# Optimization experiments

Hardware: AMD Instinct MI355X
Metric: run time of the kernel (lower is better)

Reference implementation:

```python
import jax, jax.numpy as jnp
import numpy as np

B, S, D, H = 2, 2048, 1024, 16
HD = D // H  # 64
SCALE = np.sqrt(HD).astype(np.float32)


def setup_inputs() -> dict:
    key = jax.random.key(0)
    k1, k2, k3, k4, k5, k6 = jax.random.split(key, 6)
    hidden_states = jax.random.normal(k1, (B, S, D), dtype=jnp.float32)
    attention_mask = jax.random.randint(k2, (B, 1, S, S), 0, 2) > 0  # bool
    std = 0.02
    W_qkv = jax.random.normal(k3, (D, 3 * D), dtype=jnp.float32) * std
    b_qkv = jnp.zeros((3 * D,), dtype=jnp.float32)
    W_dense = jax.random.normal(k4, (D, D), dtype=jnp.float32) * std
    b_dense = jnp.zeros((D,), dtype=jnp.float32)
    return {
        "hidden_states": hidden_states,
        "attention_mask": attention_mask,
        "W_qkv": W_qkv,
        "b_qkv": b_qkv,
        "W_dense": W_dense,
        "b_dense": b_dense,
    }


def reference(hidden_states, attention_mask, W_qkv, b_qkv, W_dense, b_dense):
    # fused QKV projection: [B,S,3D]
    qkv = hidden_states @ W_qkv + b_qkv
    q, k, v = jnp.split(qkv, 3, axis=-1)
    # split heads -> [B,H,S,hd]
    q = q.reshape(B, S, H, HD).transpose(0, 2, 1, 3)
    k = k.reshape(B, S, H, HD).transpose(0, 2, 1, 3)
    v = v.reshape(B, S, H, HD).transpose(0, 2, 1, 3)
    # scores [B,H,S,S]
    scores = jnp.einsum("bhqd,bhkd->bhqk", q, k) / SCALE
    scores = jnp.where(attention_mask, scores, jnp.float32(-50000.0))
    probs = jax.nn.softmax(scores, axis=-1)
    ctx = jnp.einsum("bhqk,bhkd->bhqd", probs, v)
    # merge heads -> [B,S,D]
    ctx = ctx.transpose(0, 2, 1, 3).reshape(B, S, D)
    return ctx @ W_dense + b_dense
```

## Files before the change

kernel.cpp:

```cpp
#include <hip/hip_runtime.h>
#include <stdint.h>

#define B_ 2
#define S_ 2048
#define D_ 1024
#define H_ 16
#define HD_ 64
#define D3_ 3072
#define KD_ 1024

typedef __attribute__((ext_vector_type(8))) __bf16 bf16x8;
typedef __attribute__((ext_vector_type(4))) float f32x4;
typedef __attribute__((ext_vector_type(16))) float f32x16;
typedef __attribute__((ext_vector_type(4))) unsigned int u32x4;

typedef const __attribute__((address_space(1))) unsigned int gu32_t;
typedef __attribute__((address_space(3))) unsigned int lu32_t;

static __device__ __forceinline__ unsigned short f2bf(float f) {
  unsigned int u = __float_as_uint(f);
  u += 0x7fffu + ((u >> 16) & 1u);
  return (unsigned short)(u >> 16);
}

static __device__ __forceinline__ void gll16(const unsigned short* g, unsigned short* l) {
  __builtin_amdgcn_global_load_lds((gu32_t*)(const void*)g, (lu32_t*)(void*)l, 16, 0, 0);
}

static __device__ __forceinline__ bf16x8 lds_read8(const unsigned short* p) {
  return *reinterpret_cast<const bf16x8*>(p);
}

static __device__ __forceinline__ unsigned int cvtpk(float lo, float hi) {
  unsigned int r;
  asm("v_cvt_pk_bf16_f32 %0, %1, %2" : "=v"(r) : "v"(lo), "v"(hi));
  return r;
}

static __device__ __forceinline__ void plswap(unsigned int& a, unsigned int& b) {
  asm("v_permlane32_swap_b32 %0, %1" : "+v"(a), "+v"(b));
}

static __device__ __forceinline__ void transpose32(const float* __restrict__ in,
                                                   unsigned short* __restrict__ out,
                                                   int K, int N, int bx, int by, int t,
                                                   float (*tsm)[33]) {
  const int k0 = by * 32, n0 = bx * 32;
  const int tx = t & 31, ty = t >> 5;
  #pragma unroll
  for (int j = 0; j < 32; j += 8) tsm[ty + j][tx] = in[(size_t)(k0 + ty + j) * N + n0 + tx];
  __syncthreads();
  #pragma unroll
  for (int j = 0; j < 32; j += 8) out[(size_t)(n0 + ty + j) * K + k0 + tx] = f2bf(tsm[tx][ty + j]);
}

__global__ void prep_kernel(const float* __restrict__ hidden, unsigned short* __restrict__ Xb,
                            const float* __restrict__ Wq, unsigned short* __restrict__ Wqt,
                            const void* __restrict__ mask,
                            unsigned long long* __restrict__ bits,
                            const float* __restrict__ Wd, unsigned short* __restrict__ Wdt) {
  __shared__ float tsm[32][33];
  __shared__ unsigned int red2[2];
  const int bid = blockIdx.x;
  const int t = threadIdx.x;
  if (bid < 4096) {
    const int i = (bid * 256 + t) * 4;
    float4 v = *reinterpret_cast<const float4*>(hidden + i);
    unsigned long long p = (unsigned long long)f2bf(v.x)
                         | ((unsigned long long)f2bf(v.y) << 16)
                         | ((unsigned long long)f2bf(v.z) << 32)
                         | ((unsigned long long)f2bf(v.w) << 48);
    *reinterpret_cast<unsigned long long*>(Xb + i) = p;
  } else if (bid < 7168) {
    const int bb = bid - 4096;
    transpose32(Wq, Wqt, KD_, D3_, bb % 96, bb / 96, t, tsm);
  } else if (bid < 8192) {
    if (t < 2) red2[t] = 0;
    __syncthreads();
    {
      const unsigned int* mw = (const unsigned int*)mask;
      unsigned int hb = 0, fl = 0;
      for (int i = t; i < 4096; i += 256) {
        unsigned int v = mw[i];
        hb |= (v & 0xFFFFFF00u);
        fl |= (v == 0x3F800000u) ? 1u : 0u;
      }
      atomicOr(&red2[0], hb);
      atomicOr(&red2[1], fl);
    }
    __syncthreads();
    const unsigned int mode = red2[1] ? 2u : (red2[0] ? 1u : 0u);
    const int lane = t & 63;
    const int nwaves = 1024 * 4;
    const int wid = ((bid - 7168) * 256 + t) >> 6;
    const int total = (B_ * S_ * S_) / 256;
    for (int wb = wid; wb < total; wb += nwaves) {
      const size_t base = (size_t)wb * 256 + lane;
      unsigned long long m0, m1, m2, m3;
      if (mode == 0) {
        const int* p = (const int*)mask;
        m0 = __ballot(p[base] != 0);       m1 = __ballot(p[base + 64] != 0);
        m2 = __ballot(p[base + 128] != 0); m3 = __ballot(p[base + 192] != 0);
      } else if (mode == 1) {
        const unsigned char* p = (const unsigned char*)mask;
        m0 = __ballot(p[base] != 0);       m1 = __ballot(p[base + 64] != 0);
        m2 = __ballot(p[base + 128] != 0); m3 = __ballot(p[base + 192] != 0);
      } else {
        const float* p = (const float*)mask;
        m0 = __ballot(p[base] != 0.f);       m1 = __ballot(p[base + 64] != 0.f);
        m2 = __ballot(p[base + 128] != 0.f); m3 = __ballot(p[base + 192] != 0.f);
      }
      if (lane < 4) {
        unsigned long long v = (lane & 1) ? m1 : m0;
        unsigned long long w2 = (lane & 1) ? m3 : m2;
        v = (lane & 2) ? w2 : v;
        bits[(size_t)wb * 4 + lane] = v;
      }
    }
  } else {
    const int bb = bid - 8192;
    transpose32(Wd, Wdt, D_, D_, bb & 31, bb >> 5, t, tsm);
  }
}

__global__ void tcvt_kernel(const float* __restrict__ in, unsigned short* __restrict__ out, int K, int N) {
  __shared__ float tsm[32][33];
  transpose32(in, out, K, N, blockIdx.x, blockIdx.y, threadIdx.x, tsm);
}

#define DSA256(BUF, MH, KC) \
  _Pragma("unroll") for (int fm_ = 0; fm_ < 4; ++fm_) \
    aq[fm_] = lds_read8(&Al[BUF][(wm * 128 + (MH) * 64 + fm_ * 16 + c16) * 64 + (KC)]);
#define DSB256(BUF, KC) \
  _Pragma("unroll") for (int fn_ = 0; fn_ < 3; ++fn_) \
    bq[fn_] = lds_read8(&Bl[BUF][(wn * 48 + fn_ * 16 + c16) * 64 + (KC)]);
#define MM256(MH) \
  __builtin_amdgcn_s_setprio(1); \
  _Pragma("unroll") for (int fm_ = 0; fm_ < 4; ++fm_) \
    _Pragma("unroll") for (int fn_ = 0; fn_ < 3; ++fn_) \
      acc[MH][fm_][fn_] = __builtin_amdgcn_mfma_f32_16x16x32_bf16(aq[fm_], bq[fn_], acc[MH][fm_][fn_], 0, 0, 0); \
  __builtin_amdgcn_s_setprio(0);
#define STA256(BUF, KT1) \
  _Pragma("unroll") for (int q_ = 0; q_ < 4; ++q_) \
    gll16(Ag + (size_t)(q_ * 64) * KD_ + (size_t)(KT1) * 64, &Al[BUF][q_ * 4096 + t * 8]);
#define STB256(BUF, KT1) \
  _Pragma("unroll") for (int q_ = 0; q_ < 3; ++q_) \
    gll16(Bg + (size_t)(q_ * 64) * KD_ + (size_t)(KT1) * 64, &Bl[BUF][q_ * 4096 + t * 8]);

__global__ __launch_bounds__(512, 2) void gemm256_kernel(
    const unsigned short* __restrict__ A,
    const unsigned short* __restrict__ Bt,
    const float* __restrict__ bias,
    unsigned short* __restrict__ Qh,
    unsigned short* __restrict__ Kh,
    unsigned short* __restrict__ Vt) {
  __shared__ unsigned short Al[2][16384];
  __shared__ unsigned short Bl[2][12288];
  const int t = threadIdx.x;
  const int lane = t & 63, w = t >> 6;
  const int g = lane >> 4, c16 = lane & 15;
  const int wm = w >> 2, wn = w & 3;

  const int wg = blockIdx.x;
  const int sw = (wg & 7) * 32 + (wg >> 3);
  const int by = sw >> 4, bx = sw & 15;
  const int m0 = by * 256, n0 = bx * 192;

  f32x4 acc[2][4][3];
  #pragma unroll
  for (int mh = 0; mh < 2; ++mh)
    #pragma unroll
    for (int fm = 0; fm < 4; ++fm)
      #pragma unroll
      for (int fn = 0; fn < 3; ++fn)
        #pragma unroll
        for (int r = 0; r < 4; ++r) acc[mh][fm][fn][r] = 0.f;

  const int srow = t >> 3;
  const int scb = (t & 7) ^ (srow & 7);
  const unsigned short* Ag = A + (size_t)(m0 + srow) * KD_ + scb * 8;
  const unsigned short* Bg = Bt + (size_t)(n0 + srow) * KD_ + scb * 8;

  const int kc0 = ((g ^ (c16 & 7)) * 8);
  const int kc1 = (((4 + g) ^ (c16 & 7)) * 8);

  bf16x8 aq[4], bq[3];

  STA256(0, 0); STB256(0, 0);
  __syncthreads();

  #pragma unroll 1
  for (int kt = 0; kt < 16; ++kt) {
    const int buf = kt & 1, nb = buf ^ 1;
    const bool st = kt < 15;
    DSA256(buf, 0, kc0); DSB256(buf, kc0);
    if (st) STA256(nb, kt + 1);
    MM256(0);
    DSA256(buf, 1, kc0);
    if (st) STB256(nb, kt + 1);
    MM256(1);
    DSA256(buf, 0, kc1); DSB256(buf, kc1);
    MM256(0);
    DSA256(buf, 1, kc1);
    MM256(1);
    __syncthreads();
  }

  #pragma unroll
  for (int mh = 0; mh < 2; ++mh) {
    #pragma unroll
    for (int fn = 0; fn < 3; ++fn) {
      const int n = n0 + wn * 48 + fn * 16 + c16;
      const float bv = bias[n];
      const int sel = n >> 10;
      const int hh = (n & 1023) >> 6;
      const int d = n & 63;
      #pragma unroll
      for (int fm = 0; fm < 4; ++fm) {
        const int m_b = m0 + wm * 128 + mh * 64 + fm * 16 + g * 4;
        const int b = m_b >> 11;
        const int s0 = m_b & 2047;
        const int bh = b * H_ + hh;
        if (sel == 2) {
          ushort4 pk;
          pk.x = f2bf(acc[mh][fm][fn][0] + bv);
          pk.y = f2bf(acc[mh][fm][fn][1] + bv);
          pk.z = f2bf(acc[mh][fm][fn][2] + bv);
          pk.w = f2bf(acc[mh][fm][fn][3] + bv);
          *reinterpret_cast<ushort4*>(&Vt[(size_t)(bh * HD_ + d) * S_ + s0]) = pk;
        } else {
          #pragma unroll
          for (int r = 0; r < 4; ++r) {
            const float v = acc[mh][fm][fn][r] + bv;
            if (sel == 0) Qh[(size_t)(bh * S_ + s0 + r) * HD_ + d] = f2bf(v * 0.18033688011112042f);
            else          Kh[(size_t)(bh * S_ + s0 + r) * HD_ + d] = f2bf(v);
          }
        }
      }
    }
  }
}

#define DDA(BUF, KC) \
  _Pragma("unroll") for (int i_ = 0; i_ < 4; ++i_) \
    aq[i_] = lds_read8(&Al[BUF][(wr * 64 + i_ * 16 + c16) * 64 + (KC)]);
#define DDB(BUF, KC) \
  _Pragma("unroll") for (int i_ = 0; i_ < 4; ++i_) \
    bq[i_] = lds_read8(&Bl[BUF][(wc * 64 + i_ * 16 + c16) * 64 + (KC)]);
#define DMM \
  __builtin_amdgcn_s_setprio(1); \
  _Pragma("unroll") for (int mi_ = 0; mi_ < 4; ++mi_) \
    _Pragma("unroll") for (int ni_ = 0; ni_ < 4; ++ni_) \
      acc[mi_][ni_] = __builtin_amdgcn_mfma_f32_16x16x32_bf16(aq[mi_], bq[ni_], acc[mi_][ni_], 0, 0, 0); \
  __builtin_amdgcn_s_setprio(0);
#define DSTA(BUF, KT1) \
  _Pragma("unroll") for (int q_ = 0; q_ < 4; ++q_) \
    gll16(Ag + (size_t)(q_ * 32) * KD_ + (size_t)(KT1) * 64, &Al[BUF][q_ * 2048 + t * 8]);
#define DSTB(BUF, KT1) \
  _Pragma("unroll") for (int q_ = 0; q_ < 4; ++q_) \
    gll16(Bg + (size_t)(q_ * 32) * KD_ + (size_t)(KT1) * 64, &Bl[BUF][q_ * 2048 + t * 8]);

__global__ __launch_bounds__(256, 2) void gemm128p_kernel(
    const unsigned short* __restrict__ A,
    const unsigned short* __restrict__ Bt,
    const float* __restrict__ bias,
    int Ndim,
    float* __restrict__ Out) {
  __shared__ unsigned short Al[2][8192];
  __shared__ unsigned short Bl[2][8192];
  const int t = threadIdx.x;
  const int lane = t & 63, w = t >> 6;
  const int g = lane >> 4, c16 = lane & 15;
  const int wr = w >> 1, wc = w & 1;

  const int wg = blockIdx.x;
  const int sw = (wg & 7) * 32 + (wg >> 3);
  const int by = sw >> 3, bx = sw & 7;
  const int m0 = by * 128, n0 = bx * 128;

  f32x4 acc[4][4];
  #pragma unroll
  for (int mi = 0; mi < 4; ++mi)
    #pragma unroll
    for (int ni = 0; ni < 4; ++ni)
      #pragma unroll
      for (int r = 0; r < 4; ++r) acc[mi][ni][r] = 0.f;

  const int srow = t >> 3;
  const int scb = (t & 7) ^ (srow & 7);
  const unsigned short* Ag = A + (size_t)(m0 + srow) * KD_ + scb * 8;
  const unsigned short* Bg = Bt + (size_t)(n0 + srow) * KD_ + scb * 8;

  const int kc0 = ((g ^ (c16 & 7)) * 8);
  const int kc1 = (((4 + g) ^ (c16 & 7)) * 8);

  bf16x8 aq[4], bq[4];

  DSTA(0, 0); DSTB(0, 0);
  __syncthreads();

  #pragma unroll 1
  for (int kt = 0; kt < 16; ++kt) {
    const int buf = kt & 1, nb = buf ^ 1;
    const bool st = kt < 15;
    DDA(buf, kc0); DDB(buf, kc0);
    if (st) DSTA(nb, kt + 1);
    DMM;
    DDA(buf, kc1); DDB(buf, kc1);
    if (st) DSTB(nb, kt + 1);
    DMM;
    __syncthreads();
  }

  #pragma unroll
  for (int ni = 0; ni < 4; ++ni) {
    const int n = n0 + wc * 64 + ni * 16 + c16;
    const float bv = bias[n];
    #pragma unroll
    for (int mi = 0; mi < 4; ++mi) {
      #pragma unroll
      for (int r = 0; r < 4; ++r) {
        const int m = m0 + wr * 64 + mi * 16 + g * 4 + r;
        Out[(size_t)m * Ndim + n] = acc[mi][ni][r] + bv;
      }
    }
  }
}

#define PPOS(r) ((((r) & 3)) + 8 * ((r) >> 2))

#define SOFTPACK(SV, WQ, FLO, FHI) do {                                         \
    float p_[16];                                                               \
    _Pragma("unroll") for (int r_ = 0; r_ < 16; ++r_) {                         \
      float e_ = __builtin_amdgcn_exp2f((SV)[r_]);                              \
      int m_;                                                                   \
      asm("v_bfe_i32 %0, %1, %2, 1" : "=v"(m_) : "v"(WQ), "i"(PPOS(r_)));       \
      p_[r_] = __uint_as_float(__float_as_uint(e_) & (unsigned int)m_);         \
    }                                                                           \
    {                                                                           \
      unsigned int a0 = cvtpk(p_[0], p_[1]),  a1 = cvtpk(p_[2], p_[3]);         \
      unsigned int b0 = cvtpk(p_[4], p_[5]),  b1 = cvtpk(p_[6], p_[7]);         \
      plswap(a0, b0); plswap(a1, b1);                                           \
      u32x4 t_; t_[0] = a0; t_[1] = a1; t_[2] = b0; t_[3] = b1;                 \
      FLO = __builtin_bit_cast(bf16x8, t_);                                     \
    }                                                                           \
    {                                                                           \
      unsigned int a0 = cvtpk(p_[8], p_[9]),   a1 = cvtpk(p_[10], p_[11]);      \
      unsigned int b0 = cvtpk(p_[12], p_[13]), b1 = cvtpk(p_[14], p_[15]);      \
      plswap(a0, b0); plswap(a1, b1);                                           \
      u32x4 t_; t_[0] = a0; t_[1] = a1; t_[2] = b0; t_[3] = b1;                 \
      FHI = __builtin_bit_cast(bf16x8, t_);                                     \
    }                                                                           \
  } while (0)

#define PROC_KT(BUF, KT, WQW) do {                                              \
    f32x16 s0_;                                                                 \
    {                                                                           \
      bf16x8 kf_ = lds_read8(&sm[vp[0] + (BUF) * 8192 + (KT) * 2048]);          \
      s0_ = __builtin_amdgcn_mfma_f32_32x32x16_bf16(kf_, qf[0], zacc, 0, 0, 0); \
    }                                                                           \
    _Pragma("unroll") for (int kc_ = 1; kc_ < 4; ++kc_) {                       \
      bf16x8 kf_ = lds_read8(&sm[vp[kc_] + (BUF) * 8192 + (KT) * 2048]);        \
      s0_ = __builtin_amdgcn_mfma_f32_32x32x16_bf16(kf_, qf[kc_], s0_, 0, 0, 0); \
    }                                                                           \
    unsigned int wq_ = (WQW) >> sh4;                                            \
    bf16x8 paL_, paH_;                                                          \
    SOFTPACK(s0_, wq_, paL_, paH_);                                             \
    rsum = __builtin_amdgcn_mfma_f32_32x32x16_bf16(paL_, ones, rsum, 0, 0, 0);  \
    rsum = __builtin_amdgcn_mfma_f32_32x32x16_bf16(paH_, ones, rsum, 0, 0, 0);  \
    {                                                                           \
      bf16x8 vf0_ = lds_read8(&sm[vp[(KT)*2 + 0] + (BUF) * 8192 + 4096]);       \
      bf16x8 vf1_ = lds_read8(&sm[vp[(KT)*2 + 0] + (BUF) * 8192 + 4096 + 2048]); \
      ctx0 = __builtin_amdgcn_mfma_f32_32x32x16_bf16(paL_, vf0_, ctx0, 0, 0, 0); \
      ctx1 = __builtin_amdgcn_mfma_f32_32x32x16_bf16(paL_, vf1_, ctx1, 0, 0, 0); \
    }                                                                           \
    {                                                                           \
      bf16x8 vf0_ = lds_read8(&sm[vp[(KT)*2 + 1] + (BUF) * 8192 + 4096]);       \
      bf16x8 vf1_ = lds_read8(&sm[vp[(KT)*2 + 1] + (BUF) * 8192 + 4096 + 2048]); \
      ctx0 = __builtin_amdgcn_mfma_f32_32x32x16_bf16(paH_, vf0_, ctx0, 0, 0, 0); \
      ctx1 = __builtin_amdgcn_mfma_f32_32x32x16_bf16(paH_, vf1_, ctx1, 0, 0, 0); \
    }                                                                           \
  } while (0)

#define STAGE_TO(DBUF) do {                                                     \
    gll16(Kg,         &sm[kvb + (DBUF) * 8192 + qc1024]);                       \
    gll16(Kg + 512,   &sm[kvb + (DBUF) * 8192 + qc1024 + 512]);                 \
    gll16(Vg,         &sm[kvb + (DBUF) * 8192 + 4096 + qc1024]);                \
    gll16(Vg + 16384, &sm[kvb + (DBUF) * 8192 + 4096 + qc1024 + 512]);          \
    Kg += 4096; Vg += 64;                                                       \
  } while (0)

#define TILE64(BUF, KB, DOSTAGE) do {                                           \
    const uint2 mw_ = *(const uint2*)(mp + 2 * (KB));                           \
    if (DOSTAGE) STAGE_TO((BUF) ^ 1);                                           \
    PROC_KT(BUF, 0, mw_.x);                                                     \
    PROC_KT(BUF, 1, mw_.y);                                                     \
    __syncthreads();                                                            \
  } while (0)

__global__ __launch_bounds__(512, 4) void flash_kernel(
    const unsigned short* __restrict__ Qh,
    const unsigned short* __restrict__ Kh,
    const unsigned short* __restrict__ Vt,
    const unsigned long long* __restrict__ mbits,
    unsigned short* __restrict__ Ctx) {
  __shared__ unsigned short sm[32768];
  const int t = threadIdx.x;
  const int lane = t & 63, w = t >> 6;
  const int hi = lane >> 5, l31 = lane & 31;
  const int grp = w >> 2, qc = w & 3;

  const int lin = blockIdx.x;
  const int swz = (lin & 7) * 64 + (lin >> 3);
  const int qt = swz & 15, bhid = swz >> 4;
  const int h = bhid & 15, b = bhid >> 4;

  const int bh = b * H_ + h;
  const int qrow = qt * 128 + qc * 32 + l31;
  const int sh4 = hi * 4;
  const int kvb = grp * 16384;
  const int qc1024 = qc * 1024;

  bf16x8 qf[4];
  {
    const unsigned short* Qr = Qh + (size_t)(bh * S_ + qrow) * HD_ + hi * 8;
    #pragma unroll
    for (int kc = 0; kc < 4; ++kc) qf[kc] = *reinterpret_cast<const bf16x8*>(Qr + kc * 16);
  }

  f32x16 ctx0, ctx1, rsum, zacc;
  #pragma unroll
  for (int i = 0; i < 16; ++i) { ctx0[i] = 0.f; ctx1[i] = 0.f; rsum[i] = 0.f; zacc[i] = 0.f; }
  bf16x8 ones;
  #pragma unroll
  for (int i = 0; i < 8; ++i) ones[i] = (__bf16)1.0f;

  int vp[4];
  #pragma unroll
  for (int c = 0; c < 4; ++c)
    vp[c] = grp * 16384 + l31 * 64 + (((2 * c + hi) ^ (l31 & 7)) * 8);

  const unsigned int* mp =
      (const unsigned int*)(mbits + (size_t)(b * S_ + qrow) * 32) + grp * 32;

  const int srw = lane >> 3;
  const int scb = (lane & 7) ^ (srw & 7);
  const unsigned short* Kg = Kh + (size_t)(bh * S_ + grp * 1024 + qc * 16 + srw) * HD_ + scb * 8;
  const unsigned short* Vg = Vt + (size_t)(bh * HD_ + qc * 16 + srw) * S_ + grp * 1024 + scb * 8;

  STAGE_TO(0);
  __syncthreads();

  #pragma unroll 1
  for (int kb = 0; kb < 16; kb += 2) {
    TILE64(0, kb, 1);
    TILE64(1, kb + 1, (kb < 14));
  }

  float* creg = (float*)sm;
  if (grp == 1) {
    float* ex = creg + qc * 3072 + lane;
    #pragma unroll
    for (int r = 0; r < 16; ++r) {
      ex[r * 64] = ctx0[r];
      ex[(16 + r) * 64] = ctx1[r];
      ex[(32 + r) * 64] = rsum[r];
    }
  }
  __syncthreads();
  if (grp == 0) {
    const float* im = creg + qc * 3072 + lane;
    #pragma unroll
    for (int r = 0; r < 16; ++r) {
      const float c0 = ctx0[r] + im[r * 64];
      const float c1 = ctx1[r] + im[(16 + r) * 64];
      const float rt = rsum[r] + im[(32 + r) * 64];
      const float iv = 1.0f / rt;
      const int sq = qt * 128 + qc * 32 + PPOS(r) + 4 * hi;
      unsigned short* op = Ctx + (size_t)(b * S_ + sq) * D_ + h * HD_ + l31;
      op[0]  = f2bf(c0 * iv);
      op[32] = f2bf(c1 * iv);
    }
  }
}

extern "C" void kernel_launch(void* const* d_in, const int* in_sizes, int n_in,
                              void* d_out, int out_size, void* d_ws, size_t ws_size,
                              hipStream_t stream) {
  const float* hidden  = (const float*)d_in[0];
  const void*  mask    = d_in[1];
  const float* W_qkv   = (const float*)d_in[2];
  const float* b_qkv   = (const float*)d_in[3];
  const float* W_dense = (const float*)d_in[4];
  const float* b_dense = (const float*)d_in[5];
  float* out = (float*)d_out;

  char* ws = (char*)d_ws;
  unsigned short* Qh   = (unsigned short*)(ws);
  unsigned short* Kh   = (unsigned short*)(ws + 8388608);
  unsigned short* Vtb  = (unsigned short*)(ws + 16777216);
  unsigned short* Xb   = (unsigned short*)(ws + 25165824);
  unsigned short* Ctx  = Xb;
  unsigned short* Wqt  = (unsigned short*)(ws + 33554432);
  unsigned long long* mbits = (unsigned long long*)(ws + 39845888);

  const bool fused = ws_size >= 44040192ull;
  unsigned short* Wdt = fused ? (unsigned short*)(ws + 41943040) : Wqt;

  prep_kernel<<<fused ? 9216 : 8192, 256, 0, stream>>>(
      hidden, Xb, W_qkv, Wqt, mask, mbits, W_dense, Wdt);

  gemm256_kernel<<<256, 512, 0, stream>>>(Xb, Wqt, b_qkv, Qh, Kh, Vtb);

  if (!fused)
    tcvt_kernel<<<dim3(D_ / 32, D_ / 32), 256, 0, stream>>>(W_dense, Wdt, D_, D_);

  flash_kernel<<<512, 512, 0, stream>>>(Qh, Kh, Vtb, mbits, Ctx);

  gemm128p_kernel<<<256, 256, 0, stream>>>(Ctx, Wdt, b_dense, D_, out);
}
```

Before: 126.9 us.

## Fuse fp32-to-bf16 conversion of hidden states into QKV GEMM A-tile loads

After: 125.7 us. No clear change (-0.9%).

```diff
diff --git a/kernel.cpp b/kernel.cpp
--- a/kernel.cpp
+++ b/kernel.cpp
@@ -54,8 +54,7 @@
   for (int j = 0; j < 32; j += 8) out[(size_t)(n0 + ty + j) * K + k0 + tx] = f2bf(tsm[tx][ty + j]);
 }
 
-__global__ void prep_kernel(const float* __restrict__ hidden, unsigned short* __restrict__ Xb,
-                            const float* __restrict__ Wq, unsigned short* __restrict__ Wqt,
+__global__ void prep_kernel(const float* __restrict__ Wq, unsigned short* __restrict__ Wqt,
                             const void* __restrict__ mask,
                             unsigned long long* __restrict__ bits,
                             const float* __restrict__ Wd, unsigned short* __restrict__ Wdt) {
@@ -63,18 +62,9 @@
   __shared__ unsigned int red2[2];
   const int bid = blockIdx.x;
   const int t = threadIdx.x;
-  if (bid < 4096) {
-    const int i = (bid * 256 + t) * 4;
-    float4 v = *reinterpret_cast<const float4*>(hidden + i);
-    unsigned long long p = (unsigned long long)f2bf(v.x)
-                         | ((unsigned long long)f2bf(v.y) << 16)
-                         | ((unsigned long long)f2bf(v.z) << 32)
-                         | ((unsigned long long)f2bf(v.w) << 48);
-    *reinterpret_cast<unsigned long long*>(Xb + i) = p;
-  } else if (bid < 7168) {
-    const int bb = bid - 4096;
-    transpose32(Wq, Wqt, KD_, D3_, bb % 96, bb / 96, t, tsm);
-  } else if (bid < 8192) {
+  if (bid < 3072) {
+    transpose32(Wq, Wqt, KD_, D3_, bid % 96, bid / 96, t, tsm);
+  } else if (bid < 4096) {
     if (t < 2) red2[t] = 0;
     __syncthreads();
     {
@@ -92,7 +82,7 @@
     const unsigned int mode = red2[1] ? 2u : (red2[0] ? 1u : 0u);
     const int lane = t & 63;
     const int nwaves = 1024 * 4;
-    const int wid = ((bid - 7168) * 256 + t) >> 6;
+    const int wid = ((bid - 3072) * 256 + t) >> 6;
     const int total = (B_ * S_ * S_) / 256;
     for (int wb = wid; wb < total; wb += nwaves) {
       const size_t base = (size_t)wb * 256 + lane;
@@ -118,7 +108,7 @@
       }
     }
   } else {
-    const int bb = bid - 8192;
+    const int bb = bid - 4096;
     transpose32(Wd, Wdt, D_, D_, bb & 31, bb >> 5, t, tsm);
   }
 }
@@ -140,15 +130,27 @@
     _Pragma("unroll") for (int fn_ = 0; fn_ < 3; ++fn_) \
       acc[MH][fm_][fn_] = __builtin_amdgcn_mfma_f32_16x16x32_bf16(aq[fm_], bq[fn_], acc[MH][fm_][fn_], 0, 0, 0); \
   __builtin_amdgcn_s_setprio(0);
-#define STA256(BUF, KT1) \
-  _Pragma("unroll") for (int q_ = 0; q_ < 4; ++q_) \
-    gll16(Ag + (size_t)(q_ * 64) * KD_ + (size_t)(KT1) * 64, &Al[BUF][q_ * 4096 + t * 8]);
+#define ALOAD256(KT1) \
+  _Pragma("unroll") for (int q_ = 0; q_ < 4; ++q_) { \
+    const float* s_ = Ag + (size_t)(q_ * 64) * KD_ + (size_t)(KT1) * 64; \
+    fA[q_][0] = *reinterpret_cast<const float4*>(s_); \
+    fA[q_][1] = *reinterpret_cast<const float4*>(s_ + 4); \
+  }
+#define AWRT256(BUF) \
+  _Pragma("unroll") for (int q_ = 0; q_ < 4; ++q_) { \
+    u32x4 pk_; \
+    pk_[0] = cvtpk(fA[q_][0].x, fA[q_][0].y); \
+    pk_[1] = cvtpk(fA[q_][0].z, fA[q_][0].w); \
+    pk_[2] = cvtpk(fA[q_][1].x, fA[q_][1].y); \
+    pk_[3] = cvtpk(fA[q_][1].z, fA[q_][1].w); \
+    *reinterpret_cast<u32x4*>(&Al[BUF][q_ * 4096 + t * 8]) = pk_; \
+  }
 #define STB256(BUF, KT1) \
   _Pragma("unroll") for (int q_ = 0; q_ < 3; ++q_) \
     gll16(Bg + (size_t)(q_ * 64) * KD_ + (size_t)(KT1) * 64, &Bl[BUF][q_ * 4096 + t * 8]);
 
 __global__ __launch_bounds__(512, 2) void gemm256_kernel(
-    const unsigned short* __restrict__ A,
+    const float* __restrict__ Af,
     const unsigned short* __restrict__ Bt,
     const float* __restrict__ bias,
     unsigned short* __restrict__ Qh,
@@ -178,23 +180,26 @@
 
   const int srow = t >> 3;
   const int scb = (t & 7) ^ (srow & 7);
-  const unsigned short* Ag = A + (size_t)(m0 + srow) * KD_ + scb * 8;
+  const float* Ag = Af + (size_t)(m0 + srow) * KD_ + scb * 8;
   const unsigned short* Bg = Bt + (size_t)(n0 + srow) * KD_ + scb * 8;
 
   const int kc0 = ((g ^ (c16 & 7)) * 8);
   const int kc1 = (((4 + g) ^ (c16 & 7)) * 8);
 
   bf16x8 aq[4], bq[3];
-
-  STA256(0, 0); STB256(0, 0);
+  float4 fA[4][2];
+
+  ALOAD256(0);
+  STB256(0, 0);
+  AWRT256(0);
   __syncthreads();
 
   #pragma unroll 1
   for (int kt = 0; kt < 16; ++kt) {
     const int buf = kt & 1, nb = buf ^ 1;
     const bool st = kt < 15;
+    if (st) ALOAD256(kt + 1);
     DSA256(buf, 0, kc0); DSB256(buf, kc0);
-    if (st) STA256(nb, kt + 1);
     MM256(0);
     DSA256(buf, 1, kc0);
     if (st) STB256(nb, kt + 1);
@@ -202,6 +207,7 @@
     DSA256(buf, 0, kc1); DSB256(buf, kc1);
     MM256(0);
     DSA256(buf, 1, kc1);
+    if (st) AWRT256(nb);
     MM256(1);
     __syncthreads();
   }
@@ -499,18 +505,17 @@
   unsigned short* Qh   = (unsigned short*)(ws);
   unsigned short* Kh   = (unsigned short*)(ws + 8388608);
   unsigned short* Vtb  = (unsigned short*)(ws + 16777216);
-  unsigned short* Xb   = (unsigned short*)(ws + 25165824);
-  unsigned short* Ctx  = Xb;
+  unsigned short* Ctx  = (unsigned short*)(ws + 25165824);
   unsigned short* Wqt  = (unsigned short*)(ws + 33554432);
   unsigned long long* mbits = (unsigned long long*)(ws + 39845888);
 
   const bool fused = ws_size >= 44040192ull;
   unsigned short* Wdt = fused ? (unsigned short*)(ws + 41943040) : Wqt;
 
-  prep_kernel<<<fused ? 9216 : 8192, 256, 0, stream>>>(
-      hidden, Xb, W_qkv, Wqt, mask, mbits, W_dense, Wdt);
-
-  gemm256_kernel<<<256, 512, 0, stream>>>(Xb, Wqt, b_qkv, Qh, Kh, Vtb);
+  prep_kernel<<<fused ? 5120 : 4096, 256, 0, stream>>>(
+      W_qkv, Wqt, mask, mbits, W_dense, Wdt);
+
+  gemm256_kernel<<<256, 512, 0, stream>>>(hidden, Wqt, b_qkv, Qh, Kh, Vtb);
 
   if (!fused)
     tcvt_kernel<<<dim3(D_ / 32, D_ / 32), 256, 0, stream>>>(W_dense, Wdt, D_, D_);
```
